# Kernel tuning notes

Measured on AMD Instinct MI355X. Metric: run time of the kernel, lower is better.

The kernel has to match this reference:

```python
import jax, jax.numpy as jnp
import numpy as np
from jax import lax

B, T, HW = 8, 32, 128
D, NH, DEPTH, DFF = 384, 6, 6, 1536
PR = PC = 4
P = PR * PC
EPS = 1e-5


def _ln(x, g, b):
    mu = x.mean(-1, keepdims=True)
    v = ((x - mu) ** 2).mean(-1, keepdims=True)
    return (x - mu) / jnp.sqrt(v + EPS) * g + b


def _conv2d(x, w, s, p):
    return lax.conv_general_dilated(x, w, (s, s), [(p, p), (p, p)],
                                    dimension_numbers=('NCHW', 'OIHW', 'NCHW'))


def _bn(x, g, b, m, v):
    inv = g / jnp.sqrt(v + EPS)
    return x * inv[:, None, None] + (b - m * inv)[:, None, None]


def _gelu(x):
    return jax.nn.gelu(x, approximate=False)


def _forward(frames, conv1_w, bn1_g, bn1_b, bn1_m, bn1_v,
             conv2_w, bn2_g, bn2_b, bn2_m, bn2_v,
             conv3_w, bn3_g, bn3_b, bn3_m, bn3_v, proj_w,
             dw_w, dw_b, pw_w, pw_b, tnorm_g, tnorm_b,
             frame_pos, patch_pos, cls_token, cls_pos,
             qkv_w, qkv_b, out_w, out_b, ln1_g, ln1_b, ln2_g, ln2_b,
             ffn_w1, ffn_b1, ffn_w2, ffn_b2,
             head_ln_g, head_ln_b, head_w1, head_b1, head_w2, head_b2):
    b, t = frames.shape[0], frames.shape[1]
    # ---- FrameEncoder (eval-mode BN) ----
    x = frames.reshape(b * t, 1, HW, HW)
    x = _gelu(_bn(_conv2d(x, conv1_w, 2, 2), bn1_g, bn1_b, bn1_m, bn1_v))
    x = _gelu(_bn(_conv2d(x, conv2_w, 2, 1), bn2_g, bn2_b, bn2_m, bn2_v))
    x = _gelu(_bn(_conv2d(x, conv3_w, 2, 1), bn3_g, bn3_b, bn3_m, bn3_v))
    n, c, hh, ww = x.shape
    # adaptive avg pool (16,16)->(4,4) is an exact 4x4 mean pool
    x = x.reshape(n, c, PR, hh // PR, PC, ww // PC).mean(axis=(3, 5))
    x = jnp.einsum('oc,nchw->nohw', proj_w[:, :, 0, 0], x)  # 1x1 conv proj
    tokens = x.reshape(n, D, P).transpose(0, 2, 1).reshape(b, t, P, D)
    # ---- TemporalConvBlock (per-patch sequences) ----
    tc = tokens.transpose(0, 2, 1, 3).reshape(b * P, t, D)
    out = tc.transpose(0, 2, 1)  # [N, D, t]
    for i, dil in enumerate((1, 2)):
        pad = dil * (3 - 1) // 2
        h = lax.conv_general_dilated(out, dw_w[i], (1,), [(pad, pad)],
                                     rhs_dilation=(dil,), feature_group_count=D,
                                     dimension_numbers=('NCH', 'OIH', 'NCH'))
        h = _gelu(h + dw_b[i][None, :, None])
        h = jnp.einsum('oi,nit->not', pw_w[i], h) + pw_b[i][None, :, None]
        out = h + out
    out = out.transpose(0, 2, 1)
    tc = _ln(out + tc, tnorm_g, tnorm_b)
    tokens = tc.reshape(b, P, t, D).transpose(0, 2, 1, 3)
    # ---- positional + cls ----
    fp = frame_pos[:t].transpose(1, 0, 2)[:, :, None, :]  # [1,t,1,D]
    pp = patch_pos[:, None, :, :]                          # [1,1,P,D]
    tok = (tokens + fp + pp).reshape(b, t * P, D)
    cls = cls_token + cls_pos
    tok = jnp.concatenate([jnp.broadcast_to(cls, (b, 1, D)), tok], axis=1)
    S = t * P + 1
    # ---- block-structured additive mask (faithful to _build_causal_mask) ----
    ids = jnp.repeat(jnp.arange(t), P)
    neg = jnp.finfo(jnp.float32).min
    base = jnp.where(ids[None, :] < ids[:, None], neg, 0.0)
    mask = jnp.zeros((S, S), jnp.float32).at[1:, 1:].set(base).at[1:, 0].set(neg)
    # ---- pre-norm transformer encoder ----
    hd = D // NH
    scale = 1.0 / jnp.sqrt(jnp.float32(hd))
    x = tok
    for i in range(DEPTH):
        h = _ln(x, ln1_g[i], ln1_b[i])
        qkv = h @ qkv_w[i].T + qkv_b[i]
        q, k, v = jnp.split(qkv, 3, axis=-1)
        q = q.reshape(b, S, NH, hd).transpose(0, 2, 1, 3)
        k = k.reshape(b, S, NH, hd).transpose(0, 2, 1, 3)
        v = v.reshape(b, S, NH, hd).transpose(0, 2, 1, 3)
        scores = jnp.einsum('bhqd,bhkd->bhqk', q, k) * scale + mask
        a = jax.nn.softmax(scores, axis=-1)
        o = jnp.einsum('bhqk,bhkd->bhqd', a, v).transpose(0, 2, 1, 3).reshape(b, S, D)
        x = x + (o @ out_w[i].T + out_b[i])
        h2 = _ln(x, ln2_g[i], ln2_b[i])
        x = x + _gelu(h2 @ ffn_w1[i].T + ffn_b1[i]) @ ffn_w2[i].T + ffn_b2[i]
    # ---- coord head ----
    pooled = x[:, 0]
    h = _ln(pooled, head_ln_g, head_ln_b)
    h = _gelu(h @ head_w1.T + head_b1)
    coords = jax.nn.sigmoid(h @ head_w2.T + head_b2)
    return coords


def setup_inputs():
    ks = iter(jax.random.split(jax.random.key(0), 64))

    def r(shape, s):
        return jax.random.normal(next(ks), shape, jnp.float32) * s

    inp = {}
    inp['frames'] = jax.random.normal(next(ks), (B, T, 1, HW, HW), jnp.float32)
    inp['conv1_w'] = r((32, 1, 5, 5), 0.2)
    inp['bn1_g'] = jnp.ones(32); inp['bn1_b'] = jnp.zeros(32)
    inp['bn1_m'] = r((32,), 0.1)
    inp['bn1_v'] = jax.random.uniform(next(ks), (32,), jnp.float32, 0.5, 1.5)
    inp['conv2_w'] = r((64, 32, 3, 3), 0.1)
    inp['bn2_g'] = jnp.ones(64); inp['bn2_b'] = jnp.zeros(64)
    inp['bn2_m'] = r((64,), 0.1)
    inp['bn2_v'] = jax.random.uniform(next(ks), (64,), jnp.float32, 0.5, 1.5)
    inp['conv3_w'] = r((128, 64, 3, 3), 0.07)
    inp['bn3_g'] = jnp.ones(128); inp['bn3_b'] = jnp.zeros(128)
    inp['bn3_m'] = r((128,), 0.1)
    inp['bn3_v'] = jax.random.uniform(next(ks), (128,), jnp.float32, 0.5, 1.5)
    inp['proj_w'] = r((D, 128, 1, 1), 0.08)
    inp['dw_w'] = r((2, D, 1, 3), 0.3)
    inp['dw_b'] = jnp.zeros((2, D))
    inp['pw_w'] = r((2, D, D), 0.05)
    inp['pw_b'] = jnp.zeros((2, D))
    inp['tnorm_g'] = jnp.ones(D); inp['tnorm_b'] = jnp.zeros(D)
    inp['frame_pos'] = r((T, 1, D), 0.02)
    inp['patch_pos'] = r((1, P, D), 0.02)
    inp['cls_token'] = jnp.zeros((1, 1, D))
    inp['cls_pos'] = r((1, 1, D), 0.02)
    inp['qkv_w'] = r((DEPTH, 3 * D, D), 0.02)
    inp['qkv_b'] = jnp.zeros((DEPTH, 3 * D))
    inp['out_w'] = r((DEPTH, D, D), 0.02)
    inp['out_b'] = jnp.zeros((DEPTH, D))
    inp['ln1_g'] = jnp.ones((DEPTH, D)); inp['ln1_b'] = jnp.zeros((DEPTH, D))
    inp['ln2_g'] = jnp.ones((DEPTH, D)); inp['ln2_b'] = jnp.zeros((DEPTH, D))
    inp['ffn_w1'] = r((DEPTH, DFF, D), 0.02)
    inp['ffn_b1'] = jnp.zeros((DEPTH, DFF))
    inp['ffn_w2'] = r((DEPTH, D, DFF), 0.02)
    inp['ffn_b2'] = jnp.zeros((DEPTH, D))
    inp['head_ln_g'] = jnp.ones(D); inp['head_ln_b'] = jnp.zeros(D)
    inp['head_w1'] = r((D, D), 0.02); inp['head_b1'] = jnp.zeros(D)
    inp['head_w2'] = r((2, D), 0.02); inp['head_b2'] = jnp.zeros(2)
    return inp


def reference(frames, conv1_w, bn1_g, bn1_b, bn1_m, bn1_v,
              conv2_w, bn2_g, bn2_b, bn2_m, bn2_v,
              conv3_w, bn3_g, bn3_b, bn3_m, bn3_v, proj_w,
              dw_w, dw_b, pw_w, pw_b, tnorm_g, tnorm_b,
              frame_pos, patch_pos, cls_token, cls_pos,
              qkv_w, qkv_b, out_w, out_b, ln1_g, ln1_b, ln2_g, ln2_b,
              ffn_w1, ffn_b1, ffn_w2, ffn_b2,
              head_ln_g, head_ln_b, head_w1, head_b1, head_w2, head_b2):
    return _forward(frames, conv1_w, bn1_g, bn1_b, bn1_m, bn1_v,
                    conv2_w, bn2_g, bn2_b, bn2_m, bn2_v,
                    conv3_w, bn3_g, bn3_b, bn3_m, bn3_v, proj_w,
                    dw_w, dw_b, pw_w, pw_b, tnorm_g, tnorm_b,
                    frame_pos, patch_pos, cls_token, cls_pos,
                    qkv_w, qkv_b, out_w, out_b, ln1_g, ln1_b, ln2_g, ln2_b,
                    ffn_w1, ffn_b1, ffn_w2, ffn_b2,
                    head_ln_g, head_ln_b, head_w1, head_b1, head_w2, head_b2)
```

## Files before the change

kernel.cpp:

```cpp
#include <hip/hip_runtime.h>
#include <hip/hip_fp16.h>
#include <cstddef>

#define EPSV 1e-5f

typedef _Float16 f16;
typedef _Float16 f16x8 __attribute__((ext_vector_type(8)));
typedef float f32x4v __attribute__((ext_vector_type(4)));

__device__ __forceinline__ float gelu_f(float x) {
    return 0.5f * x * (1.0f + erff(x * 0.7071067811865476f));
}

__device__ __forceinline__ float gelu_fast(float x) {
    float y = 0.7978845608f * (x + 0.044715f * x * x * x);
    y = fminf(fmaxf(y, -10.f), 10.f);
    float e = __expf(2.f * y);
    float t = (e - 1.f) / (e + 1.f);
    return 0.5f * x * (1.f + t);
}

__global__ __launch_bounds__(256) void cvt_all_kernel(
    const float* __restrict__ p0, const float* __restrict__ p1,
    const float* __restrict__ p2, const float* __restrict__ p3,
    const float* __restrict__ p4, const float* __restrict__ p5,
    f16* __restrict__ dst)
{
    const int n = 10960896;
    for (int i = blockIdx.x * 256 + threadIdx.x; i < n; i += gridDim.x * 256) {
        const float* s; int off;
        if      (i <   49152) { s = p0; off = i; }
        else if (i <  344064) { s = p1; off = i -   49152; }
        else if (i < 2998272) { s = p2; off = i -  344064; }
        else if (i < 3883008) { s = p3; off = i - 2998272; }
        else if (i < 7421952) { s = p4; off = i - 3883008; }
        else                  { s = p5; off = i - 7421952; }
        dst[i] = (f16)s[off];
    }
}

__global__ __launch_bounds__(256) void conv_w_reorder_kernel(
    const float* __restrict__ w, f16* __restrict__ out, int CO, int CI)
{
    int n = CO * CI * 9;
    for (int i = blockIdx.x * 256 + threadIdx.x; i < n; i += gridDim.x * 256) {
        int t = i % 9; int r = i / 9;
        int ci = r % CI; int co = r / CI;
        out[(size_t)co * CI * 9 + t * CI + ci] = (f16)w[i];
    }
}

__global__ __launch_bounds__(256) void conv1_wave_kernel(
    const float* __restrict__ in, const float* __restrict__ w,
    const float* __restrict__ g, const float* __restrict__ bt,
    const float* __restrict__ mn, const float* __restrict__ vr,
    f16* __restrict__ out)
{
    __shared__ float inp[35][37];
    int bid = blockIdx.x;
    int n = bid >> 4; int tile = bid & 15;
    int ty0 = (tile >> 2) * 16, tx0 = (tile & 3) * 16;
    int t = threadIdx.x;
    const float* ip = in + (size_t)n * 16384;
    for (int e = t; e < 35 * 36; e += 256) {
        int r = e / 36, c = e - r * 36;
        int iy = ty0 * 2 - 2 + r, ix = tx0 * 2 - 2 + c;
        inp[r][c] = ((unsigned)iy < 128u && (unsigned)ix < 128u) ? ip[iy * 128 + ix] : 0.f;
    }
    __syncthreads();
    int wv = __builtin_amdgcn_readfirstlane(t >> 6);
    int lane = t & 63;
    int cobase = wv * 8;
    float sc[8], be[8];
    #pragma unroll
    for (int c = 0; c < 8; c++) {
        int co = cobase + c;
        float iv = g[co] * rsqrtf(vr[co] + EPSV);
        sc[c] = iv; be[c] = bt[co] - mn[co] * iv;
    }
    #pragma unroll
    for (int pix = 0; pix < 4; pix++) {
        int p = pix * 64 + lane;
        int py = p >> 4, px = p & 15;
        float r0[25];
        #pragma unroll
        for (int ky = 0; ky < 5; ky++)
            #pragma unroll
            for (int kx = 0; kx < 5; kx++)
                r0[ky * 5 + kx] = inp[2 * py + ky][2 * px + kx];
        f16 o[8];
        #pragma unroll
        for (int c = 0; c < 8; c++) {
            const float* wp = w + (cobase + c) * 25;
            float acc = 0.f;
            #pragma unroll
            for (int k = 0; k < 25; k++) acc += wp[k] * r0[k];
            o[c] = (f16)gelu_fast(acc * sc[c] + be[c]);
        }
        size_t ob = (((size_t)n * 64 + ty0 + py) * 64 + tx0 + px) * 32 + cobase;
        *(uint4*)(out + ob) = *(uint4*)o;
    }
}

template<int CI, int HI, int CO>
__global__ __launch_bounds__(256) void convg_kernel(
    const f16* __restrict__ in, const f16* __restrict__ wr_,
    const float* __restrict__ g, const float* __restrict__ bt,
    const float* __restrict__ mn, const float* __restrict__ vr,
    f16* __restrict__ out)
{
    constexpr int HO = HI / 2;
    constexpr int HOB = (HO == 32) ? 5 : 4;
    constexpr int K = 9 * CI;
    __shared__ __align__(16) f16 As[64 * 40];
    __shared__ __align__(16) f16 Bs[64 * 40];
    int tid = threadIdx.x;
    int bm = blockIdx.x * 64;
    int bn = blockIdx.y * 64;
    int lrow = tid >> 2, lseg = tid & 3;
    int w = tid >> 6, lane = tid & 63;
    int wr = (w >> 1) * 32, wc = (w & 1) * 32;
    int l15 = lane & 15, l4 = lane >> 4;
    int gp = bm + lrow;
    int pn = gp >> (2 * HOB);
    int prem = gp & ((1 << (2 * HOB)) - 1);
    int oy = prem >> HOB, ox = prem & (HO - 1);

    f32x4v zero = {0.f, 0.f, 0.f, 0.f};
    f32x4v acc[2][2];
    acc[0][0] = zero; acc[0][1] = zero; acc[1][0] = zero; acc[1][1] = zero;

    for (int k0 = 0; k0 < K; k0 += 32) {
        int tap = k0 / CI;
        int cio = k0 - tap * CI;
        int ky = tap / 3, kx = tap - ky * 3;
        int iy = oy * 2 - 1 + ky, ix = ox * 2 - 1 + kx;
        uint4 av = make_uint4(0u, 0u, 0u, 0u);
        if ((unsigned)iy < (unsigned)HI && (unsigned)ix < (unsigned)HI)
            av = *(const uint4*)(in + (((size_t)(pn * HI + iy)) * HI + ix) * CI + cio + lseg * 8);
        *(uint4*)(&As[lrow * 40 + lseg * 8]) = av;
        uint4 bv = *(const uint4*)(wr_ + (size_t)(bn + lrow) * K + k0 + lseg * 8);
        *(uint4*)(&Bs[lrow * 40 + lseg * 8]) = bv;
        __syncthreads();
        f16x8 a0 = *(const f16x8*)(&As[(wr + l15) * 40 + l4 * 8]);
        f16x8 a1 = *(const f16x8*)(&As[(wr + 16 + l15) * 40 + l4 * 8]);
        f16x8 b0 = *(const f16x8*)(&Bs[(wc + l15) * 40 + l4 * 8]);
        f16x8 b1 = *(const f16x8*)(&Bs[(wc + 16 + l15) * 40 + l4 * 8]);
        acc[0][0] = __builtin_amdgcn_mfma_f32_16x16x32_f16(a0, b0, acc[0][0], 0, 0, 0);
        acc[0][1] = __builtin_amdgcn_mfma_f32_16x16x32_f16(a0, b1, acc[0][1], 0, 0, 0);
        acc[1][0] = __builtin_amdgcn_mfma_f32_16x16x32_f16(a1, b0, acc[1][0], 0, 0, 0);
        acc[1][1] = __builtin_amdgcn_mfma_f32_16x16x32_f16(a1, b1, acc[1][1], 0, 0, 0);
        __syncthreads();
    }
    float inv[2], beta[2];
    #pragma unroll
    for (int ni = 0; ni < 2; ni++) {
        int col = bn + wc + ni * 16 + l15;
        float iv = g[col] * rsqrtf(vr[col] + EPSV);
        inv[ni] = iv; beta[ni] = bt[col] - mn[col] * iv;
    }
    #pragma unroll
    for (int mi = 0; mi < 2; mi++) {
        #pragma unroll
        for (int q = 0; q < 4; q++) {
            int pixel = bm + wr + mi * 16 + l4 * 4 + q;
            #pragma unroll
            for (int ni = 0; ni < 2; ni++) {
                int col = bn + wc + ni * 16 + l15;
                float v = acc[mi][ni][q] * inv[ni] + beta[ni];
                out[(size_t)pixel * CO + col] = (f16)gelu_fast(v);
            }
        }
    }
}

__global__ __launch_bounds__(256) void poolh_kernel(
    const f16* __restrict__ in, f16* __restrict__ out, int NC)
{
    int idx = blockIdx.x * 256 + threadIdx.x;
    if (idx >= NC * 16 * 16) return;
    int cc = idx & 15; int npl = idx >> 4;
    int c0 = cc * 8;
    int n = npl >> 4; int p = npl & 15;
    int ph = p >> 2, pw = p & 3;
    const f16* base = in + (((size_t)(n * 16 + ph * 4)) * 16 + pw * 4) * 128 + c0;
    float s[8] = {};
    #pragma unroll
    for (int dy = 0; dy < 4; dy++)
        #pragma unroll
        for (int dx = 0; dx < 4; dx++) {
            f16x8 v = *(const f16x8*)(base + (dy * 16 + dx) * 128);
            #pragma unroll
            for (int u = 0; u < 8; u++) s[u] += (float)v[u];
        }
    f16* op = out + (size_t)npl * 128 + c0;
    #pragma unroll
    for (int u = 0; u < 8; u++) op[u] = (f16)(s[u] * 0.0625f);
}

template<int OUTF16, int ACT, int VTRANS>
__global__ __launch_bounds__(256) void gemm_k64_kernel(
    const f16* __restrict__ A, const f16* __restrict__ B,
    const float* __restrict__ bias, const float* __restrict__ res,
    void* __restrict__ Cv, f16* __restrict__ vT, int M, int N, int K, int nrow)
{
    __shared__ __align__(16) f16 As[64 * 72];
    __shared__ __align__(16) f16 Bs[64 * 72];
    int nb = gridDim.x;
    int q = nb >> 3, r = nb & 7;
    int xcd = blockIdx.x & 7, pos = blockIdx.x >> 3;
    int logical = (xcd < r ? xcd * (q + 1) : r * (q + 1) + (xcd - r) * q) + pos;
    int brow = logical % nrow, bcol = logical / nrow;
    int bm = brow * 64, bn = bcol * 64;

    int tid = threadIdx.x;
    int lrow = tid >> 2, lseg = (tid & 3) * 16;
    int w = tid >> 6, lane = tid & 63;
    int wr = (w >> 1) * 32, wc = (w & 1) * 32;
    int l15 = lane & 15, l4 = lane >> 4;
    f32x4v zero = {0.f, 0.f, 0.f, 0.f};
    f32x4v acc[2][2];
    acc[0][0] = zero; acc[0][1] = zero; acc[1][0] = zero; acc[1][1] = zero;

    int arow = bm + lrow;
    bool aok = (arow < M);
    const f16* ap = A + (size_t)arow * K + lseg;
    const f16* bp = B + (size_t)(bn + lrow) * K + lseg;

    uint4 ra0 = make_uint4(0u,0u,0u,0u), ra1 = ra0, rb0, rb1;
    if (aok) { ra0 = *(const uint4*)(ap); ra1 = *(const uint4*)(ap + 8); }
    rb0 = *(const uint4*)(bp); rb1 = *(const uint4*)(bp + 8);

    int nt = K >> 6;
    for (int t = 0; t < nt; t++) {
        __syncthreads();
        *(uint4*)(&As[lrow * 72 + lseg])     = ra0;
        *(uint4*)(&As[lrow * 72 + lseg + 8]) = ra1;
        *(uint4*)(&Bs[lrow * 72 + lseg])     = rb0;
        *(uint4*)(&Bs[lrow * 72 + lseg + 8]) = rb1;
        if (t + 1 < nt) {
            int k0 = (t + 1) << 6;
            if (aok) { ra0 = *(const uint4*)(ap + k0); ra1 = *(const uint4*)(ap + k0 + 8); }
            rb0 = *(const uint4*)(bp + k0); rb1 = *(const uint4*)(bp + k0 + 8);
        }
        __syncthreads();
        #pragma unroll
        for (int s = 0; s < 2; s++) {
            f16x8 a0 = *(const f16x8*)(&As[(wr + l15) * 72 + s * 32 + l4 * 8]);
            f16x8 a1 = *(const f16x8*)(&As[(wr + 16 + l15) * 72 + s * 32 + l4 * 8]);
            f16x8 b0 = *(const f16x8*)(&Bs[(wc + l15) * 72 + s * 32 + l4 * 8]);
            f16x8 b1 = *(const f16x8*)(&Bs[(wc + 16 + l15) * 72 + s * 32 + l4 * 8]);
            acc[0][0] = __builtin_amdgcn_mfma_f32_16x16x32_f16(a0, b0, acc[0][0], 0, 0, 0);
            acc[0][1] = __builtin_amdgcn_mfma_f32_16x16x32_f16(a0, b1, acc[0][1], 0, 0, 0);
            acc[1][0] = __builtin_amdgcn_mfma_f32_16x16x32_f16(a1, b0, acc[1][0], 0, 0, 0);
            acc[1][1] = __builtin_amdgcn_mfma_f32_16x16x32_f16(a1, b1, acc[1][1], 0, 0, 0);
        }
    }

    if (VTRANS && bn >= 768) {
        __syncthreads();
        f16* tile = As;
        #pragma unroll
        for (int mi = 0; mi < 2; mi++)
            #pragma unroll
            for (int qq = 0; qq < 4; qq++) {
                int rl = wr + mi * 16 + l4 * 4 + qq;
                #pragma unroll
                for (int ni = 0; ni < 2; ni++) {
                    int dl = wc + ni * 16 + l15;
                    float v = acc[mi][ni][qq] + bias[bn + dl];
                    tile[dl * 66 + rl] = (f16)v;
                }
            }
        __syncthreads();
        int h = (bn - 768) >> 6;
        int j = tid & 63, dbase = tid >> 6;
        int trow = bm + j;
        if (trow < M) {
            int b = trow / 513;
            int jj = trow - b * 513;
            f16* vb = vT + ((size_t)(b * 6 + h) * 64) * 576 + jj;
            #pragma unroll
            for (int it = 0; it < 16; it++) {
                int d = dbase * 16 + it;
                vb[(size_t)d * 576] = tile[d * 66 + j];
            }
        }
        return;
    }
    #pragma unroll
    for (int mi = 0; mi < 2; mi++) {
        #pragma unroll
        for (int qq = 0; qq < 4; qq++) {
            int row = bm + wr + mi * 16 + l4 * 4 + qq;
            if (row >= M) continue;
            #pragma unroll
            for (int ni = 0; ni < 2; ni++) {
                int col = bn + wc + ni * 16 + l15;
                float v = acc[mi][ni][qq];
                if (bias) v += bias[col];
                if (ACT == 1) v = gelu_fast(v);
                if (res) v += res[(size_t)row * N + col];
                if (OUTF16) ((f16*)Cv)[(size_t)row * N + col] = (f16)v;
                else ((float*)Cv)[(size_t)row * N + col] = v;
            }
        }
    }
}

__global__ __launch_bounds__(256) void tok2tc_kernel(
    const float* __restrict__ in, float* __restrict__ out)
{
    int idx = blockIdx.x * 256 + threadIdx.x;
    if (idx >= 8 * 32 * 16 * 384) return;
    int d = idx % 384; int t2 = idx / 384;
    int p = t2 & 15; t2 >>= 4;
    int t = t2 & 31; int b = t2 >> 5;
    out[(((size_t)(b * 16 + p) * 32 + t) * 384) + d] = in[idx];
}

__global__ __launch_bounds__(256) void dwconv_kernel(
    const float* __restrict__ in, const float* __restrict__ w,
    const float* __restrict__ bias, f16* __restrict__ out, int dil)
{
    int idx = blockIdx.x * 256 + threadIdx.x;
    if (idx >= 128 * 32 * 384) return;
    int d = idx % 384; int t = (idx / 384) & 31; int s = idx / (384 * 32);
    const float* ip = in + (size_t)s * 32 * 384 + d;
    float acc = bias[d];
    #pragma unroll
    for (int k = 0; k < 3; k++) {
        int tt = t + (k - 1) * dil;
        if ((unsigned)tt < 32u) acc += w[d * 3 + k] * ip[tt * 384];
    }
    out[idx] = (f16)gelu_fast(acc);
}

__global__ __launch_bounds__(256) void ln_wave_kernel(
    const float* __restrict__ in,
    const float* __restrict__ g, const float* __restrict__ b,
    f16* __restrict__ out, int rows)
{
    int w = threadIdx.x >> 6, lane = threadIdx.x & 63;
    int row = blockIdx.x * 4 + w;
    if (row >= rows) return;
    const float* ip = in + (size_t)row * 384;
    float x[6]; float s = 0.f, s2 = 0.f;
    #pragma unroll
    for (int k = 0; k < 6; k++) {
        float v = ip[lane + 64 * k];
        x[k] = v; s += v; s2 += v * v;
    }
    #pragma unroll
    for (int off = 1; off < 64; off <<= 1) {
        s += __shfl_xor(s, off); s2 += __shfl_xor(s2, off);
    }
    float mu = s * (1.f / 384.f);
    float var = s2 * (1.f / 384.f) - mu * mu;
    float rs = rsqrtf(var + EPSV);
    #pragma unroll
    for (int k = 0; k < 6; k++) {
        int c = lane + 64 * k;
        out[(size_t)row * 384 + c] = (f16)((x[k] - mu) * rs * g[c] + b[c]);
    }
}

__global__ __launch_bounds__(128) void build_x_kernel(
    const float* __restrict__ mix, const float* __restrict__ tc,
    const float* __restrict__ tg, const float* __restrict__ tb,
    const float* __restrict__ fpos, const float* __restrict__ ppos,
    float* __restrict__ x)
{
    int row = blockIdx.x;
    int t = row & 31; int bp = row >> 5;
    int p = bp & 15; int b = bp >> 4;
    int tid = threadIdx.x;
    const float* ip = mix + (size_t)row * 384;
    const float* ip2 = tc + (size_t)row * 384;
    __shared__ float red[128], red2[128];
    float v[3]; float s = 0.f, s2 = 0.f;
    #pragma unroll
    for (int j = 0; j < 3; j++) {
        float val = ip[tid + 128 * j] + ip2[tid + 128 * j];
        v[j] = val; s += val; s2 += val * val;
    }
    red[tid] = s; red2[tid] = s2; __syncthreads();
    for (int off = 64; off >= 1; off >>= 1) {
        if (tid < off) { red[tid] += red[tid + off]; red2[tid] += red2[tid + off]; }
        __syncthreads();
    }
    float mu = red[0] * (1.f / 384.f);
    float var = red2[0] * (1.f / 384.f) - mu * mu;
    float rs = rsqrtf(var + EPSV);
    size_t xbase = ((size_t)b * 513 + 1 + t * 16 + p) * 384;
    #pragma unroll
    for (int j = 0; j < 3; j++) {
        int c = tid + 128 * j;
        float y = (v[j] - mu) * rs * tg[c] + tb[c] + fpos[t * 384 + c] + ppos[p * 384 + c];
        x[xbase + c] = y;
    }
}

__global__ __launch_bounds__(256) void cls_kernel(
    const float* __restrict__ ct, const float* __restrict__ cp, float* __restrict__ x)
{
    int idx = blockIdx.x * 256 + threadIdx.x;
    if (idx >= 8 * 384) return;
    int c = idx % 384; int b = idx / 384;
    x[(size_t)b * 513 * 384 + c] = ct[c] + cp[c];
}

__global__ __launch_bounds__(256) void fattn_split_kernel(
    const f16* __restrict__ qkv, const f16* __restrict__ vT,
    float* __restrict__ Op, float* __restrict__ ml)
{
    __shared__ __align__(16) f16 Pl[4][16][72];
    int qt = blockIdx.x;
    int bh = blockIdx.y; int h = bh % 6; int b = bh / 6;
    int half = blockIdx.z;
    int tid = threadIdx.x;
    int w = tid >> 6, lane = tid & 63;
    int l15 = lane & 15, g = lane >> 4;
    int q0w = qt * 64 + w * 16;
    if (q0w > 512) return;
    const size_t RS = 1152;
    const f16* qbase = qkv + (size_t)b * 513 * RS + h * 64;
    const f16* kbase = qbase + 384;
    const f16* vtb = vT + (size_t)bh * 64 * 576;

    f16x8 qf[2];
    {
        int qrow = q0w + l15; if (qrow > 512) qrow = 512;
        const f16* qp = qbase + (size_t)qrow * RS + g * 8;
        qf[0] = *(const f16x8*)(qp);
        qf[1] = *(const f16x8*)(qp + 32);
    }

    f32x4v zero = {0.f, 0.f, 0.f, 0.f};
    f32x4v O[4]; float m[4], l[4];
    #pragma unroll
    for (int i = 0; i < 4; i++) { O[i] = zero; m[i] = -INFINITY; l[i] = 0.f; }

    int jt0 = 0;
    if (q0w > 0) { int fmin = (q0w - 1) >> 4; jt0 = (fmin * 16 + 1) >> 6; }

    int jrow[4];
    #pragma unroll
    for (int jf = 0; jf < 4; jf++) jrow[jf] = jf * 16 + l15;

    auto loadK = [&](int j0, f16x8* kr) {
        #pragma unroll
        for (int s = 0; s < 2; s++)
            #pragma unroll
            for (int jf = 0; jf < 4; jf++) {
                int j = j0 + jrow[jf]; if (j > 512) j = 512;
                kr[s * 4 + jf] = *(const f16x8*)(kbase + (size_t)j * RS + s * 32 + g * 8);
            }
    };

    int jt = jt0 + half;
    f16x8 kreg[8];
    if (jt < 9) loadK(jt * 64, kreg);

    for (; jt < 9; jt += 2) {
        int j0 = jt * 64;
        f16x8 vreg[8];
        #pragma unroll
        for (int s = 0; s < 2; s++)
            #pragma unroll
            for (int df = 0; df < 4; df++)
                vreg[s * 4 + df] = *(const f16x8*)(vtb + (size_t)(df * 16 + l15) * 576 + j0 + s * 32 + g * 8);
        f32x4v S[4];
        #pragma unroll
        for (int jf = 0; jf < 4; jf++) S[jf] = zero;
        #pragma unroll
        for (int s = 0; s < 2; s++)
            #pragma unroll
            for (int jf = 0; jf < 4; jf++)
                S[jf] = __builtin_amdgcn_mfma_f32_16x16x32_f16(qf[s], kreg[s * 4 + jf], S[jf], 0, 0, 0);
        f16x8 knext[8];
        if (jt + 2 < 9) loadK((jt + 2) * 64, knext);
        float pj[4][4];
        #pragma unroll
        for (int r = 0; r < 4; r++) {
            int qi = q0w + 4 * g + r;
            int fi = (qi == 0) ? -1 : ((qi - 1) >> 4);
            float mx = -INFINITY;
            #pragma unroll
            for (int jf = 0; jf < 4; jf++) {
                int j = j0 + jrow[jf];
                bool valid = (qi < 513) && (j < 513) &&
                             !((qi != 0) && ((j == 0) || (((j - 1) >> 4) < fi)));
                float sv = valid ? S[jf][r] * 0.125f : -INFINITY;
                pj[jf][r] = sv;
                mx = fmaxf(mx, sv);
            }
            mx = fmaxf(mx, __shfl_xor(mx, 1));
            mx = fmaxf(mx, __shfl_xor(mx, 2));
            mx = fmaxf(mx, __shfl_xor(mx, 4));
            mx = fmaxf(mx, __shfl_xor(mx, 8));
            float mn = fmaxf(m[r], mx);
            float alpha = (m[r] == -INFINITY) ? 0.f : __expf(m[r] - mn);
            float ls = 0.f;
            #pragma unroll
            for (int jf = 0; jf < 4; jf++) {
                float p = (pj[jf][r] == -INFINITY) ? 0.f : __expf(pj[jf][r] - mn);
                pj[jf][r] = p; ls += p;
            }
            ls += __shfl_xor(ls, 1); ls += __shfl_xor(ls, 2);
            ls += __shfl_xor(ls, 4); ls += __shfl_xor(ls, 8);
            l[r] = alpha * l[r] + ls;
            m[r] = mn;
            #pragma unroll
            for (int df = 0; df < 4; df++) O[df][r] *= alpha;
        }
        #pragma unroll
        for (int jf = 0; jf < 4; jf++)
            #pragma unroll
            for (int r = 0; r < 4; r++)
                Pl[w][4 * g + r][jf * 16 + l15] = (f16)pj[jf][r];
        #pragma unroll
        for (int s = 0; s < 2; s++) {
            f16x8 pf = *(const f16x8*)(&Pl[w][l15][s * 32 + g * 8]);
            #pragma unroll
            for (int df = 0; df < 4; df++)
                O[df] = __builtin_amdgcn_mfma_f32_16x16x32_f16(pf, vreg[s * 4 + df], O[df], 0, 0, 0);
        }
        #pragma unroll
        for (int i = 0; i < 8; i++) kreg[i] = knext[i];
    }

    int rowbase = half * 24624 + bh * 513;
    #pragma unroll
    for (int r = 0; r < 4; r++) {
        int qi = q0w + 4 * g + r;
        if (qi > 512) continue;
        size_t ro = (size_t)(rowbase + qi);
        #pragma unroll
        for (int df = 0; df < 4; df++)
            Op[ro * 64 + df * 16 + l15] = O[df][r];
        if (l15 == 0) {
            ml[ro * 2 + 0] = m[r];
            ml[ro * 2 + 1] = l[r];
        }
    }
}

__global__ __launch_bounds__(256) void attn_combine_kernel(
    const float* __restrict__ Op, const float* __restrict__ ml,
    f16* __restrict__ ob)
{
    int row = blockIdx.x * 4 + (threadIdx.x >> 6);
    if (row >= 24624) return;
    int lane = threadIdx.x & 63;
    int bh = row / 513, qi = row - bh * 513;
    int b = bh / 6, h = bh - b * 6;
    float m0 = ml[(size_t)row * 2], l0 = ml[(size_t)row * 2 + 1];
    float m1 = ml[((size_t)24624 + row) * 2], l1 = ml[((size_t)24624 + row) * 2 + 1];
    float mm = fmaxf(m0, m1);
    float a0 = (m0 == -INFINITY) ? 0.f : __expf(m0 - mm);
    float a1 = (m1 == -INFINITY) ? 0.f : __expf(m1 - mm);
    float lden = l0 * a0 + l1 * a1;
    float o0 = Op[(size_t)row * 64 + lane];
    float o1 = Op[((size_t)24624 + row) * 64 + lane];
    float o = (o0 * a0 + o1 * a1) / lden;
    ob[((size_t)(b * 513 + qi)) * 384 + h * 64 + lane] = (f16)o;
}

__global__ __launch_bounds__(384) void head_kernel(
    const float* __restrict__ x, const float* __restrict__ lg, const float* __restrict__ lb,
    const float* __restrict__ w1, const float* __restrict__ b1,
    const float* __restrict__ w2, const float* __restrict__ b2,
    float* __restrict__ out)
{
    int b = blockIdx.x; int t = threadIdx.x;
    __shared__ float hs[384], h1[384];
    __shared__ float rs[6], rs2[6];
    const float* xp = x + (size_t)b * 513 * 384;
    float v = xp[t];
    float s = v, s2 = v * v;
    #pragma unroll
    for (int off = 32; off >= 1; off >>= 1) {
        s += __shfl_down(s, off); s2 += __shfl_down(s2, off);
    }
    if ((t & 63) == 0) { rs[t >> 6] = s; rs2[t >> 6] = s2; }
    __syncthreads();
    float S = 0.f, S2 = 0.f;
    #pragma unroll
    for (int i = 0; i < 6; i++) { S += rs[i]; S2 += rs2[i]; }
    float mu = S * (1.f / 384.f);
    float var = S2 * (1.f / 384.f) - mu * mu;
    float rstd = rsqrtf(var + EPSV);
    hs[t] = (v - mu) * rstd * lg[t] + lb[t];
    __syncthreads();
    const float* wr = w1 + (size_t)t * 384;
    float acc = b1[t];
    for (int c = 0; c < 384; c += 4) {
        float4 w4 = *reinterpret_cast<const float4*>(wr + c);
        acc += w4.x * hs[c] + w4.y * hs[c + 1] + w4.z * hs[c + 2] + w4.w * hs[c + 3];
    }
    h1[t] = gelu_f(acc);
    __syncthreads();
    float p0 = h1[t] * w2[t], p1 = h1[t] * w2[384 + t];
    #pragma unroll
    for (int off = 32; off >= 1; off >>= 1) {
        p0 += __shfl_down(p0, off); p1 += __shfl_down(p1, off);
    }
    if ((t & 63) == 0) { rs[t >> 6] = p0; rs2[t >> 6] = p1; }
    __syncthreads();
    if (t == 0) {
        float a0 = b2[0], a1 = b2[1];
        #pragma unroll
        for (int i = 0; i < 6; i++) { a0 += rs[i]; a1 += rs2[i]; }
        out[b * 2 + 0] = 1.f / (1.f + expf(-a0));
        out[b * 2 + 1] = 1.f / (1.f + expf(-a1));
    }
}

static inline int cdiv(int a, int b) { return (a + b - 1) / b; }

extern "C" void kernel_launch(void* const* d_in, const int* in_sizes, int n_in,
                              void* d_out, int out_size, void* d_ws, size_t ws_size,
                              hipStream_t stream)
{
    const float* frames  = (const float*)d_in[0];
    const float* conv1_w = (const float*)d_in[1];
    const float* bn1_g = (const float*)d_in[2]; const float* bn1_b = (const float*)d_in[3];
    const float* bn1_m = (const float*)d_in[4]; const float* bn1_v = (const float*)d_in[5];
    const float* conv2_w = (const float*)d_in[6];
    const float* bn2_g = (const float*)d_in[7]; const float* bn2_b = (const float*)d_in[8];
    const float* bn2_m = (const float*)d_in[9]; const float* bn2_v = (const float*)d_in[10];
    const float* conv3_w = (const float*)d_in[11];
    const float* bn3_g = (const float*)d_in[12]; const float* bn3_b = (const float*)d_in[13];
    const float* bn3_m = (const float*)d_in[14]; const float* bn3_v = (const float*)d_in[15];
    const float* proj_w = (const float*)d_in[16];
    const float* dw_w = (const float*)d_in[17]; const float* dw_b = (const float*)d_in[18];
    const float* pw_w = (const float*)d_in[19]; const float* pw_b = (const float*)d_in[20];
    const float* tnorm_g = (const float*)d_in[21]; const float* tnorm_b = (const float*)d_in[22];
    const float* frame_pos = (const float*)d_in[23];
    const float* patch_pos = (const float*)d_in[24];
    const float* cls_token = (const float*)d_in[25];
    const float* cls_pos = (const float*)d_in[26];
    const float* qkv_w = (const float*)d_in[27]; const float* qkv_b = (const float*)d_in[28];
    const float* out_w = (const float*)d_in[29]; const float* out_b = (const float*)d_in[30];
    const float* ln1_g = (const float*)d_in[31]; const float* ln1_b = (const float*)d_in[32];
    const float* ln2_g = (const float*)d_in[33]; const float* ln2_b = (const float*)d_in[34];
    const float* ffn_w1 = (const float*)d_in[35]; const float* ffn_b1 = (const float*)d_in[36];
    const float* ffn_w2 = (const float*)d_in[37]; const float* ffn_b2 = (const float*)d_in[38];
    const float* head_ln_g = (const float*)d_in[39]; const float* head_ln_b = (const float*)d_in[40];
    const float* head_w1 = (const float*)d_in[41]; const float* head_b1 = (const float*)d_in[42];
    const float* head_w2 = (const float*)d_in[43]; const float* head_b2 = (const float*)d_in[44];
    (void)in_sizes; (void)n_in; (void)out_size; (void)ws_size;

    char* base = (char*)d_ws;
    size_t off = 0;
    auto alloc = [&](size_t bytes) { void* p = base + off; off = (off + bytes + 255) & ~(size_t)255; return p; };

    f16* wtotal = (f16*)alloc((size_t)10960896 * 2);
    f16* projw16 = wtotal;
    f16* pw16    = wtotal + 49152;
    f16* qkvw16  = wtotal + 344064;
    f16* outw16  = wtotal + 2998272;
    f16* f1w16   = wtotal + 3883008;
    f16* f2w16   = wtotal + 7421952;
    f16* c2w16   = (f16*)alloc((size_t)64 * 288 * 2);
    f16* c3w16   = (f16*)alloc((size_t)128 * 576 * 2);
    float* tokens = (float*)alloc((size_t)4096 * 384 * 4);
    f16* pooled   = (f16*)alloc((size_t)4096 * 128 * 2);
    f16* c1h = (f16*)alloc((size_t)64 * 64 * 64 * 32 * 2);
    f16* c2h = (f16*)alloc((size_t)64 * 32 * 32 * 64 * 2);
    f16* c3h = (f16*)alloc((size_t)64 * 16 * 16 * 128 * 2);
    float* tc = (float*)alloc((size_t)4096 * 384 * 4);
    float* mA = (float*)alloc((size_t)4096 * 384 * 4);
    float* mB = (float*)alloc((size_t)4096 * 384 * 4);
    f16*   mh = (f16*)alloc((size_t)4096 * 384 * 2);
    float* xb   = (float*)alloc((size_t)8 * 513 * 384 * 4);
    f16*   hb   = (f16*)alloc((size_t)8 * 513 * 384 * 2);
    f16*   qkvb = (f16*)alloc((size_t)8 * 513 * 1152 * 2);
    f16*   vTb  = (f16*)alloc((size_t)48 * 64 * 576 * 2);
    f16*   ob   = (f16*)alloc((size_t)8 * 513 * 384 * 2);
    f16*   ffb  = (f16*)alloc((size_t)8 * 513 * 1536 * 2);
    float* Opart = (float*)alloc((size_t)2 * 24624 * 64 * 4);
    float* mlpart = (float*)alloc((size_t)2 * 24624 * 2 * 4);

    cvt_all_kernel<<<4096, 256, 0, stream>>>(
        proj_w, pw_w, qkv_w, out_w, ffn_w1, ffn_w2, wtotal);
    conv_w_reorder_kernel<<<cdiv(64 * 288, 256), 256, 0, stream>>>(conv2_w, c2w16, 64, 32);
    conv_w_reorder_kernel<<<cdiv(128 * 576, 256), 256, 0, stream>>>(conv3_w, c3w16, 128, 64);

    for (int ch = 0; ch < 4; ch++) {
        const float* fch = frames + (size_t)ch * 64 * 16384;
        conv1_wave_kernel<<<64 * 16, 256, 0, stream>>>(
            fch, conv1_w, bn1_g, bn1_b, bn1_m, bn1_v, c1h);
        convg_kernel<32, 64, 64><<<dim3(1024, 1), 256, 0, stream>>>(
            c1h, c2w16, bn2_g, bn2_b, bn2_m, bn2_v, c2h);
        convg_kernel<64, 32, 128><<<dim3(256, 2), 256, 0, stream>>>(
            c2h, c3w16, bn3_g, bn3_b, bn3_m, bn3_v, c3h);
        poolh_kernel<<<64, 256, 0, stream>>>(c3h, pooled + (size_t)ch * 1024 * 128, 64);
    }
    gemm_k64_kernel<0, 0, 0><<<384, 256, 0, stream>>>(
        pooled, projw16, nullptr, nullptr, tokens, nullptr, 4096, 384, 128, 64);

    tok2tc_kernel<<<cdiv(8 * 32 * 16 * 384, 256), 256, 0, stream>>>(tokens, tc);
    hipMemcpyAsync(mA, tc, (size_t)4096 * 384 * sizeof(float), hipMemcpyDeviceToDevice, stream);
    float* cur = mA; float* alt = mB;
    for (int it = 0; it < 2; it++) {
        int dil = (it == 0) ? 1 : 2;
        dwconv_kernel<<<cdiv(128 * 32 * 384, 256), 256, 0, stream>>>(
            cur, dw_w + (size_t)it * 384 * 3, dw_b + (size_t)it * 384, mh, dil);
        gemm_k64_kernel<0, 0, 0><<<384, 256, 0, stream>>>(
            mh, pw16 + (size_t)it * 384 * 384, pw_b + (size_t)it * 384, cur,
            alt, nullptr, 4096, 384, 384, 64);
        float* tmp = cur; cur = alt; alt = tmp;
    }

    build_x_kernel<<<128 * 32, 128, 0, stream>>>(
        cur, tc, tnorm_g, tnorm_b, frame_pos, patch_pos, xb);
    cls_kernel<<<cdiv(8 * 384, 256), 256, 0, stream>>>(cls_token, cls_pos, xb);

    const int M = 8 * 513;
    const int NR = cdiv(M, 64);
    for (int l = 0; l < 6; l++) {
        ln_wave_kernel<<<cdiv(M, 4), 256, 0, stream>>>(xb,
            ln1_g + (size_t)l * 384, ln1_b + (size_t)l * 384, hb, M);
        gemm_k64_kernel<1, 0, 1><<<NR * 18, 256, 0, stream>>>(
            hb, qkvw16 + (size_t)l * 1152 * 384, qkv_b + (size_t)l * 1152,
            nullptr, qkvb, vTb, M, 1152, 384, NR);
        fattn_split_kernel<<<dim3(9, 48, 2), 256, 0, stream>>>(qkvb, vTb, Opart, mlpart);
        attn_combine_kernel<<<cdiv(24624, 4), 256, 0, stream>>>(Opart, mlpart, ob);
        gemm_k64_kernel<0, 0, 0><<<NR * 6, 256, 0, stream>>>(
            ob, outw16 + (size_t)l * 384 * 384, out_b + (size_t)l * 384,
            xb, xb, nullptr, M, 384, 384, NR);
        ln_wave_kernel<<<cdiv(M, 4), 256, 0, stream>>>(xb,
            ln2_g + (size_t)l * 384, ln2_b + (size_t)l * 384, hb, M);
        gemm_k64_kernel<1, 1, 0><<<NR * 24, 256, 0, stream>>>(
            hb, f1w16 + (size_t)l * 1536 * 384, ffn_b1 + (size_t)l * 1536,
            nullptr, ffb, nullptr, M, 1536, 384, NR);
        gemm_k64_kernel<0, 0, 0><<<NR * 6, 256, 0, stream>>>(
            ffb, f2w16 + (size_t)l * 384 * 1536, ffn_b2 + (size_t)l * 384,
            xb, xb, nullptr, M, 384, 1536, NR);
    }

    head_kernel<<<8, 384, 0, stream>>>(
        xb, head_ln_g, head_ln_b, head_w1, head_b1, head_w2, head_b2, (float*)d_out);
}
```

Baseline: 948.0 us.

## Prefetch conv tiles, split attention three ways, batch stem, drop memcpy

The implicit-GEMM conv kernel now loads the next K tile into registers while the current tile is computed, which needs one barrier per step at a different point. Attention is split three ways along keys instead of two, and the combine kernel merges three partials. The four-chunk stem loop becomes single launches over all 256 frames, using a larger scratch region that aliases later buffers. The temporal block reads tc directly, which removes a device-to-device memcpy. Together these cut launch count and expose more parallelism, at the cost of more scratch memory and extra partial-result traffic.

```diff
diff --git a/kernel.cpp b/kernel.cpp
--- a/kernel.cpp
+++ b/kernel.cpp
@@ -130,17 +130,24 @@
     f32x4v acc[2][2];
     acc[0][0] = zero; acc[0][1] = zero; acc[1][0] = zero; acc[1][1] = zero;
 
-    for (int k0 = 0; k0 < K; k0 += 32) {
+    auto loadTile = [&](int k0, uint4& av, uint4& bv) {
         int tap = k0 / CI;
         int cio = k0 - tap * CI;
         int ky = tap / 3, kx = tap - ky * 3;
         int iy = oy * 2 - 1 + ky, ix = ox * 2 - 1 + kx;
-        uint4 av = make_uint4(0u, 0u, 0u, 0u);
+        av = make_uint4(0u, 0u, 0u, 0u);
         if ((unsigned)iy < (unsigned)HI && (unsigned)ix < (unsigned)HI)
             av = *(const uint4*)(in + (((size_t)(pn * HI + iy)) * HI + ix) * CI + cio + lseg * 8);
-        *(uint4*)(&As[lrow * 40 + lseg * 8]) = av;
-        uint4 bv = *(const uint4*)(wr_ + (size_t)(bn + lrow) * K + k0 + lseg * 8);
-        *(uint4*)(&Bs[lrow * 40 + lseg * 8]) = bv;
+        bv = *(const uint4*)(wr_ + (size_t)(bn + lrow) * K + k0 + lseg * 8);
+    };
+
+    uint4 ra, rb;
+    loadTile(0, ra, rb);
+    for (int k0 = 0; k0 < K; k0 += 32) {
+        __syncthreads();
+        *(uint4*)(&As[lrow * 40 + lseg * 8]) = ra;
+        *(uint4*)(&Bs[lrow * 40 + lseg * 8]) = rb;
+        if (k0 + 32 < K) loadTile(k0 + 32, ra, rb);
         __syncthreads();
         f16x8 a0 = *(const f16x8*)(&As[(wr + l15) * 40 + l4 * 8]);
         f16x8 a1 = *(const f16x8*)(&As[(wr + 16 + l15) * 40 + l4 * 8]);
@@ -150,7 +157,6 @@
         acc[0][1] = __builtin_amdgcn_mfma_f32_16x16x32_f16(a0, b1, acc[0][1], 0, 0, 0);
         acc[1][0] = __builtin_amdgcn_mfma_f32_16x16x32_f16(a1, b0, acc[1][0], 0, 0, 0);
         acc[1][1] = __builtin_amdgcn_mfma_f32_16x16x32_f16(a1, b1, acc[1][1], 0, 0, 0);
-        __syncthreads();
     }
     float inv[2], beta[2];
     #pragma unroll
@@ -417,7 +423,7 @@
     __shared__ __align__(16) f16 Pl[4][16][72];
     int qt = blockIdx.x;
     int bh = blockIdx.y; int h = bh % 6; int b = bh / 6;
-    int half = blockIdx.z;
+    int third = blockIdx.z;
     int tid = threadIdx.x;
     int w = tid >> 6, lane = tid & 63;
     int l15 = lane & 15, g = lane >> 4;
@@ -458,11 +464,11 @@
             }
     };
 
-    int jt = jt0 + half;
+    int jt = jt0 + third;
     f16x8 kreg[8];
     if (jt < 9) loadK(jt * 64, kreg);
 
-    for (; jt < 9; jt += 2) {
+    for (; jt < 9; jt += 3) {
         int j0 = jt * 64;
         f16x8 vreg[8];
         #pragma unroll
@@ -479,7 +485,7 @@
             for (int jf = 0; jf < 4; jf++)
                 S[jf] = __builtin_amdgcn_mfma_f32_16x16x32_f16(qf[s], kreg[s * 4 + jf], S[jf], 0, 0, 0);
         f16x8 knext[8];
-        if (jt + 2 < 9) loadK((jt + 2) * 64, knext);
+        if (jt + 3 < 9) loadK((jt + 3) * 64, knext);
         float pj[4][4];
         #pragma unroll
         for (int r = 0; r < 4; r++) {
@@ -530,7 +536,7 @@
         for (int i = 0; i < 8; i++) kreg[i] = knext[i];
     }
 
-    int rowbase = half * 24624 + bh * 513;
+    int rowbase = third * 24624 + bh * 513;
     #pragma unroll
     for (int r = 0; r < 4; r++) {
         int qi = q0w + 4 * g + r;
@@ -555,16 +561,21 @@
     int lane = threadIdx.x & 63;
     int bh = row / 513, qi = row - bh * 513;
     int b = bh / 6, h = bh - b * 6;
-    float m0 = ml[(size_t)row * 2], l0 = ml[(size_t)row * 2 + 1];
-    float m1 = ml[((size_t)24624 + row) * 2], l1 = ml[((size_t)24624 + row) * 2 + 1];
-    float mm = fmaxf(m0, m1);
-    float a0 = (m0 == -INFINITY) ? 0.f : __expf(m0 - mm);
-    float a1 = (m1 == -INFINITY) ? 0.f : __expf(m1 - mm);
-    float lden = l0 * a0 + l1 * a1;
-    float o0 = Op[(size_t)row * 64 + lane];
-    float o1 = Op[((size_t)24624 + row) * 64 + lane];
-    float o = (o0 * a0 + o1 * a1) / lden;
-    ob[((size_t)(b * 513 + qi)) * 384 + h * 64 + lane] = (f16)o;
+    float mv[3], lv[3], mm = -INFINITY;
+    #pragma unroll
+    for (int s = 0; s < 3; s++) {
+        mv[s] = ml[((size_t)s * 24624 + row) * 2];
+        lv[s] = ml[((size_t)s * 24624 + row) * 2 + 1];
+        mm = fmaxf(mm, mv[s]);
+    }
+    float onum = 0.f, lden = 0.f;
+    #pragma unroll
+    for (int s = 0; s < 3; s++) {
+        float a = (mv[s] == -INFINITY) ? 0.f : __expf(mv[s] - mm);
+        lden += lv[s] * a;
+        onum += Op[((size_t)s * 24624 + row) * 64 + lane] * a;
+    }
+    ob[((size_t)(b * 513 + qi)) * 384 + h * 64 + lane] = (f16)(onum / lden);
 }
 
 __global__ __launch_bounds__(384) void head_kernel(
@@ -667,9 +678,13 @@
     f16* c3w16   = (f16*)alloc((size_t)128 * 576 * 2);
     float* tokens = (float*)alloc((size_t)4096 * 384 * 4);
     f16* pooled   = (f16*)alloc((size_t)4096 * 128 * 2);
-    f16* c1h = (f16*)alloc((size_t)64 * 64 * 64 * 32 * 2);
-    f16* c2h = (f16*)alloc((size_t)64 * 32 * 32 * 64 * 2);
-    f16* c3h = (f16*)alloc((size_t)64 * 16 * 16 * 128 * 2);
+
+    size_t ustart = off;
+    f16* c1h = (f16*)alloc((size_t)256 * 64 * 64 * 32 * 2);
+    f16* c2h = (f16*)alloc((size_t)256 * 32 * 32 * 64 * 2);
+    f16* c3h = (f16*)alloc((size_t)256 * 16 * 16 * 128 * 2);
+    size_t uend_stem = off;
+    off = ustart;
     float* tc = (float*)alloc((size_t)4096 * 384 * 4);
     float* mA = (float*)alloc((size_t)4096 * 384 * 4);
     float* mB = (float*)alloc((size_t)4096 * 384 * 4);
@@ -680,42 +695,37 @@
     f16*   vTb  = (f16*)alloc((size_t)48 * 64 * 576 * 2);
     f16*   ob   = (f16*)alloc((size_t)8 * 513 * 384 * 2);
     f16*   ffb  = (f16*)alloc((size_t)8 * 513 * 1536 * 2);
-    float* Opart = (float*)alloc((size_t)2 * 24624 * 64 * 4);
-    float* mlpart = (float*)alloc((size_t)2 * 24624 * 2 * 4);
+    float* Opart = (float*)alloc((size_t)3 * 24624 * 64 * 4);
+    float* mlpart = (float*)alloc((size_t)3 * 24624 * 2 * 4);
+    if (off < uend_stem) off = uend_stem;
 
     cvt_all_kernel<<<4096, 256, 0, stream>>>(
         proj_w, pw_w, qkv_w, out_w, ffn_w1, ffn_w2, wtotal);
     conv_w_reorder_kernel<<<cdiv(64 * 288, 256), 256, 0, stream>>>(conv2_w, c2w16, 64, 32);
     conv_w_reorder_kernel<<<cdiv(128 * 576, 256), 256, 0, stream>>>(conv3_w, c3w16, 128, 64);
 
-    for (int ch = 0; ch < 4; ch++) {
-        const float* fch = frames + (size_t)ch * 64 * 16384;
-        conv1_wave_kernel<<<64 * 16, 256, 0, stream>>>(
-            fch, conv1_w, bn1_g, bn1_b, bn1_m, bn1_v, c1h);
-        convg_kernel<32, 64, 64><<<dim3(1024, 1), 256, 0, stream>>>(
-            c1h, c2w16, bn2_g, bn2_b, bn2_m, bn2_v, c2h);
-        convg_kernel<64, 32, 128><<<dim3(256, 2), 256, 0, stream>>>(
-            c2h, c3w16, bn3_g, bn3_b, bn3_m, bn3_v, c3h);
-        poolh_kernel<<<64, 256, 0, stream>>>(c3h, pooled + (size_t)ch * 1024 * 128, 64);
-    }
+    conv1_wave_kernel<<<256 * 16, 256, 0, stream>>>(
+        frames, conv1_w, bn1_g, bn1_b, bn1_m, bn1_v, c1h);
+    convg_kernel<32, 64, 64><<<dim3(4096, 1), 256, 0, stream>>>(
+        c1h, c2w16, bn2_g, bn2_b, bn2_m, bn2_v, c2h);
+    convg_kernel<64, 32, 128><<<dim3(1024, 2), 256, 0, stream>>>(
+        c2h, c3w16, bn3_g, bn3_b, bn3_m, bn3_v, c3h);
+    poolh_kernel<<<256, 256, 0, stream>>>(c3h, pooled, 256);
     gemm_k64_kernel<0, 0, 0><<<384, 256, 0, stream>>>(
         pooled, projw16, nullptr, nullptr, tokens, nullptr, 4096, 384, 128, 64);
 
     tok2tc_kernel<<<cdiv(8 * 32 * 16 * 384, 256), 256, 0, stream>>>(tokens, tc);
-    hipMemcpyAsync(mA, tc, (size_t)4096 * 384 * sizeof(float), hipMemcpyDeviceToDevice, stream);
-    float* cur = mA; float* alt = mB;
-    for (int it = 0; it < 2; it++) {
-        int dil = (it == 0) ? 1 : 2;
-        dwconv_kernel<<<cdiv(128 * 32 * 384, 256), 256, 0, stream>>>(
-            cur, dw_w + (size_t)it * 384 * 3, dw_b + (size_t)it * 384, mh, dil);
-        gemm_k64_kernel<0, 0, 0><<<384, 256, 0, stream>>>(
-            mh, pw16 + (size_t)it * 384 * 384, pw_b + (size_t)it * 384, cur,
-            alt, nullptr, 4096, 384, 384, 64);
-        float* tmp = cur; cur = alt; alt = tmp;
-    }
+    dwconv_kernel<<<cdiv(128 * 32 * 384, 256), 256, 0, stream>>>(
+        tc, dw_w, dw_b, mh, 1);
+    gemm_k64_kernel<0, 0, 0><<<384, 256, 0, stream>>>(
+        mh, pw16, pw_b, tc, mA, nullptr, 4096, 384, 384, 64);
+    dwconv_kernel<<<cdiv(128 * 32 * 384, 256), 256, 0, stream>>>(
+        mA, dw_w + 384 * 3, dw_b + 384, mh, 2);
+    gemm_k64_kernel<0, 0, 0><<<384, 256, 0, stream>>>(
+        mh, pw16 + 384 * 384, pw_b + 384, mA, mB, nullptr, 4096, 384, 384, 64);
 
     build_x_kernel<<<128 * 32, 128, 0, stream>>>(
-        cur, tc, tnorm_g, tnorm_b, frame_pos, patch_pos, xb);
+        mB, tc, tnorm_g, tnorm_b, frame_pos, patch_pos, xb);
     cls_kernel<<<cdiv(8 * 384, 256), 256, 0, stream>>>(cls_token, cls_pos, xb);
 
     const int M = 8 * 513;
@@ -726,7 +736,7 @@
         gemm_k64_kernel<1, 0, 1><<<NR * 18, 256, 0, stream>>>(
             hb, qkvw16 + (size_t)l * 1152 * 384, qkv_b + (size_t)l * 1152,
             nullptr, qkvb, vTb, M, 1152, 384, NR);
-        fattn_split_kernel<<<dim3(9, 48, 2), 256, 0, stream>>>(qkvb, vTb, Opart, mlpart);
+        fattn_split_kernel<<<dim3(9, 48, 3), 256, 0, stream>>>(qkvb, vTb, Opart, mlpart);
         attn_combine_kernel<<<cdiv(24624, 4), 256, 0, stream>>>(Opart, mlpart, ob);
         gemm_k64_kernel<0, 0, 0><<<NR * 6, 256, 0, stream>>>(
             ob, outw16 + (size_t)l * 384 * 384, out_b + (size_t)l * 384,
```

Result: faster. 869.6 us (-8.3%).
